# Kernel optimization log

Measured on AMD Instinct MI355X. Metric: run time of the kernel, lower is better.

## Reference

```python
import jax, jax.numpy as jnp
import numpy as np

C = 64          # num_channels
NB = 8          # num_bessel
NE = 10         # num_elements
N_NODES = 20000
N_EDGES = 320000

def _silu_norm():
    # e3nn normalize2mom constant for silu: 1/sqrt(E[silu(Z)^2]), Z~N(0,1)
    x, w = np.polynomial.hermite.hermgauss(100)
    z = np.sqrt(2.0) * x
    f = z / (1.0 + np.exp(-z))
    m2 = float(np.sum(w * f * f) / np.sqrt(np.pi))
    return np.float32(1.0 / np.sqrt(m2))

C_SILU = _silu_norm()
SQRT3 = np.float32(np.sqrt(3.0))
SQRT2 = np.float32(np.sqrt(2.0))
INV_SQRT_C = np.float32(1.0 / np.sqrt(C))
INV_SQRT_2C = np.float32(1.0 / np.sqrt(2 * C))
INV_SQRT_3C = np.float32(1.0 / np.sqrt(3 * C))
INV_SQRT_NB = np.float32(1.0 / np.sqrt(NB))
INV_SQRT_64 = np.float32(1.0 / np.sqrt(64.0))


def setup_inputs() -> dict:
    key = jax.random.key(0)
    ks = jax.random.split(key, 22)
    n = lambda k, s: jax.random.normal(k, s, dtype=jnp.float32)
    return {
        "node_feats": n(ks[0], (N_NODES, 4 * C)),
        "edge_feats": jax.random.uniform(ks[1], (N_EDGES, NB), dtype=jnp.float32),
        "edge_attrs": n(ks[2], (N_EDGES, 4)),
        "iedges": jax.random.randint(ks[3], (N_EDGES,), 0, N_NODES),
        "jedges": jax.random.randint(ks[4], (N_EDGES,), 0, N_NODES),
        "atomic_numbers": jax.random.randint(ks[5], (N_NODES,), 0, NE),
        "Wup0": n(ks[6], (C, C)), "Wup1": n(ks[7], (C, C)),
        "Wm1": n(ks[8], (NB, 64)), "Wm2": n(ks[9], (64, 64)),
        "Wm3": n(ks[10], (64, 64)), "Wm4": n(ks[11], (64, 5 * C)),
        "Wl0": n(ks[12], (2 * C, C)), "Wl1": n(ks[13], (3 * C, C)),
        "Ws0c1": n(ks[14], (NE, 1, C)), "Ws0c2": n(ks[15], (NE, 2, C)),
        "Ws0c3": n(ks[16], (NE, 2, C)),
        "Ws1c1": n(ks[17], (NE, 1, C)), "Ws1c2": n(ks[18], (NE, 1, C)),
        "Ws1c3": n(ks[19], (NE, 2, C)),
        "Wp0": n(ks[20], (C, C)), "Wp1": n(ks[21], (C, C)),
    }


def reference(node_feats, edge_feats, edge_attrs, iedges, jedges, atomic_numbers,
              Wup0, Wup1, Wm1, Wm2, Wm3, Wm4, Wl0, Wl1,
              Ws0c1, Ws0c2, Ws0c3, Ws1c1, Ws1c2, Ws1c3, Wp0, Wp1):
    Nn = node_feats.shape[0]
    # split irreps: C scalars (0e) then C vectors (1e), channel-major layout
    s = node_feats[:, :C]                       # (N, C)
    v = node_feats[:, C:].reshape(Nn, C, 3)     # (N, C, 3)

    # linear_up: per-l channel mixing, fan-in normalized (e3nn o3.Linear)
    s = (s @ Wup0) * INV_SQRT_C
    v = jnp.einsum('ncm,ck->nkm', v, Wup1) * INV_SQRT_C

    # conv_tp_weights: e3nn FullyConnectedNet [8,64,64,64,5C] with silu
    h = jax.nn.silu(edge_feats @ (Wm1 * INV_SQRT_NB)) * C_SILU
    h = jax.nn.silu(h @ (Wm2 * INV_SQRT_64)) * C_SILU
    h = jax.nn.silu(h @ (Wm3 * INV_SQRT_64)) * C_SILU
    tpw = h @ (Wm4 * INV_SQRT_64)               # (E, 5C)

    # gather sender node features per edge
    xs = s[iedges]                              # (E, C)
    xv = v[iedges]                              # (E, C, 3)
    eas = edge_attrs[:, 0:1]                    # (E, 1) scalar edge attr
    eav = edge_attrs[:, 1:4]                    # (E, 3) vector edge attr

    # 5 uvu CG paths (component-normalized e3nn TensorProduct):
    wa, wb = tpw[:, 0:C], tpw[:, C:2 * C]
    wc, wd, we = tpw[:, 2 * C:3 * C], tpw[:, 3 * C:4 * C], tpw[:, 4 * C:5 * C]
    m0 = wa * xs * eas                                              # 0e x 0e -> 0e
    m1 = wb * jnp.einsum('ecm,em->ec', xv, eav) / SQRT3             # 1e x 1e -> 0e
    m2 = (wc * xs)[:, :, None] * eav[:, None, :]                    # 0e x 1e -> 1e
    m3 = (wd * eas)[:, :, None] * xv                                # 1e x 0e -> 1e
    m4 = we[:, :, None] * jnp.cross(xv, eav[:, None, :]) / SQRT2    # 1e x 1e -> 1e

    # scatter-sum messages to receiver nodes
    msg_s = jax.ops.segment_sum(jnp.concatenate([m0, m1], axis=1), jedges, num_segments=Nn)        # (N, 2C)
    msg_v = jax.ops.segment_sum(jnp.concatenate([m2, m3, m4], axis=1), jedges, num_segments=Nn)    # (N, 3C, 3)

    # linear: middle irreps (2C x 0e + 3C x 1e) -> C x (0e + 1e)
    s2 = (msg_s @ Wl0) * INV_SQRT_2C            # (N, C)
    v2 = jnp.einsum('ncm,ck->nkm', msg_v, Wl1) * INV_SQRT_3C  # (N, C, 3)

    # symmetric (ACE/MACE) contraction, correlation=3, element-dependent weights
    w01 = Ws0c1[atomic_numbers, 0]              # (N, C)
    w02 = Ws0c2[atomic_numbers]                 # (N, 2, C)
    w03 = Ws0c3[atomic_numbers]                 # (N, 2, C)
    w11 = Ws1c1[atomic_numbers, 0]
    w12 = Ws1c2[atomic_numbers, 0]
    w13 = Ws1c3[atomic_numbers]
    vv = jnp.sum(v2 * v2, axis=-1)              # (N, C) = |v|^2 per channel
    out_s = (w01 * s2 + w02[:, 0] * s2 * s2 + w02[:, 1] * vv / SQRT3
             + w03[:, 0] * s2 * s2 * s2 + w03[:, 1] * s2 * vv / SQRT3)
    coef_v = w11 + w12 * s2 + w13[:, 0] * s2 * s2 + w13[:, 1] * vv / SQRT3
    out_v = coef_v[:, :, None] * v2             # (N, C, 3)

    # linearproduct
    so = (out_s @ Wp0) * INV_SQRT_C
    vo = jnp.einsum('ncm,ck->nkm', out_v, Wp1) * INV_SQRT_C
    return jnp.concatenate([so, vo.reshape(Nn, 3 * C)], axis=1)   # (N, 4C)
```

## Files before the change

### kernel.cpp

```cpp
#include <hip/hip_runtime.h>


typedef unsigned short u16;
typedef unsigned int u32;
typedef __attribute__((ext_vector_type(8))) short bf16x8;
typedef __attribute__((ext_vector_type(4))) float f32x4;

#define CW_UP0 0
#define CW_UP1 4096
#define CW_M1  8192
#define CW_M2  8704
#define CW_M3  12800
#define CW_M4  16896
#define CW_L0  37376
#define CW_L1  45568
#define CW_P0  57856
#define CW_P1  61952
#define CW_S01 66048
#define CW_S02 66688
#define CW_S03 67968
#define CW_S11 69248
#define CW_S12 69888
#define CW_S13 70528
#define CW_TOTAL 71808

#define C_SILU     1.6765224f
#define INV_SQRT3  0.57735027f
#define INV_SQRT2  0.70710678f
#define SC_L1      0.35355339f
#define SC_L234    0.125f

#define HSTRIDE 68
#define NFRAG   60

__device__ __forceinline__ float b2f(u16 u) {
  union { u32 i; float f; } x; x.i = ((u32)u) << 16; return x.f;
}
__device__ __forceinline__ u16 f2b(float f) {
  union { float f; u32 i; } x; x.f = f;
  u32 i = x.i;
  u32 r = (i + 0x7fffu + ((i >> 16) & 1u)) >> 16;
  return (u16)r;
}
__device__ __forceinline__ u32 pack2(float a, float b) {
  return (u32)f2b(a) | ((u32)f2b(b) << 16);
}
__device__ __forceinline__ u32 pack_hl(float y) {
  u16 h = f2b(y);
  float r = y - b2f(h);
  u16 lo = f2b(r);
  return ((u32)h << 16) | (u32)lo;
}
__device__ __forceinline__ float ldf(const void* p, size_t i, int f32) {
  return f32 ? ((const float*)p)[i] : b2f(((const u16*)p)[i]);
}
__device__ __forceinline__ float silu_n(float x) {
  return C_SILU * x / (1.0f + __expf(-x));
}
__device__ __forceinline__ bf16x8 as_bf16x8(uint4 v) {
  union { uint4 u; bf16x8 b; } x; x.u = v; return x.b;
}

__global__ void k_detect(const void* nf, int* flag) {
  __shared__ int cnt;
  if (threadIdx.x == 0) cnt = 0;
  __syncthreads();
  const u16* p = (const u16*)nf;
  int wild = 0;
  for (int i = threadIdx.x; i < 4096; i += 256) {
    float ax = fabsf(b2f(p[i]));
    if (!(ax <= 1e10f) || (ax != 0.f && ax < 1e-10f)) wild++;
  }
  atomicAdd(&cnt, wild);
  __syncthreads();
  if (threadIdx.x == 0) *flag = (cnt > 100) ? 1 : 0;
}

struct WPtrs { const void* p[16]; };

__global__ __launch_bounds__(256) void k_prep(WPtrs wp, float* __restrict__ cw,
                                              const int* __restrict__ flagp) {
  const int   sizes[16]  = {4096,4096,512,4096,4096,20480,8192,12288,4096,4096,
                            640,1280,1280,640,640,1280};
  const float scales[16] = {0.125f,0.125f,0.35355339f,0.125f,0.125f,0.125f,
                            0.08838835f,0.07216878f,0.125f,0.125f,
                            1.f,1.f,1.f,1.f,1.f,1.f};
  const int f32 = *flagp;
  int gid = blockIdx.x * 256 + threadIdx.x;
  if (gid >= CW_TOTAL) return;
  int off = gid, seg = 0;
  while (off >= sizes[seg]) { off -= sizes[seg]; seg++; }
  cw[gid] = ldf(wp.p[seg], off, f32) * scales[seg];
}

__global__ __launch_bounds__(256) void k_prepB(
    const void* __restrict__ wm1, const void* __restrict__ wm2,
    const void* __restrict__ wm3, const void* __restrict__ wm4,
    u16* __restrict__ bwH, u16* __restrict__ bwL,
    const int* __restrict__ flagp) {
  const int f32 = *flagp;
  int gid = blockIdx.x * 256 + threadIdx.x;
  if (gid >= NFRAG * 512) return;
  int f = gid >> 9, idx = gid & 511;
  int l = idx >> 3, j = idx & 7;
  int q = l >> 4, col16 = l & 15;
  float v = 0.f;
  if (f < 4) {
    int k = q * 8 + j, n = f * 16 + col16;
    if (k < 8) v = ldf(wm1, (size_t)k * 64 + n, f32);
  } else if (f < 20) {
    const void* w = (f < 12) ? wm2 : wm3;
    int t = (f < 12) ? f - 4 : f - 12;
    int n = (t >> 1) * 16 + col16, ks = t & 1;
    int k = ks * 32 + q * 8 + j;
    v = ldf(w, (size_t)k * 64 + n, f32);
  } else {
    int t = f - 20;
    int n = (t >> 1) * 16 + col16, ks = t & 1;
    int k = ks * 32 + q * 8 + j;
    v = ldf(wm4, (size_t)k * 320 + n, f32);
  }
  u16 hi = f2b(v);
  u16 lo = f2b(v - b2f(hi));
  size_t o = (size_t)f * 512 + (size_t)l * 8 + j;
  bwH[o] = hi;
  bwL[o] = lo;
}

__global__ __launch_bounds__(256) void k_hist(const int* __restrict__ je,
                                              int* __restrict__ deg, int nE) {
  int e = blockIdx.x * 256 + threadIdx.x;
  if (e < nE) atomicAdd(&deg[je[e]], 1);
}

__global__ __launch_bounds__(256) void k_scan(const int* __restrict__ deg,
                                              int* __restrict__ offs,
                                              int* __restrict__ cursor, int nN) {
  __shared__ int part[256];
  int t = threadIdx.x;
  int per = (nN + 255) / 256;
  int lo = t * per, hi = (t + 1) * per; if (hi > nN) hi = nN;
  int s = 0;
  for (int i = lo; i < hi; i++) s += deg[i];
  part[t] = s;
  __syncthreads();
  if (t == 0) {
    int run = 0;
    for (int i = 0; i < 256; i++) { int v = part[i]; part[i] = run; run += v; }
    offs[nN] = run;
  }
  __syncthreads();
  int run = part[t];
  for (int i = lo; i < hi; i++) {
    offs[i] = run; cursor[i] = run; run += deg[i];
  }
}

__global__ __launch_bounds__(256) void k_scatter(const int* __restrict__ je,
                                                 int* __restrict__ cursor,
                                                 int* __restrict__ eidx, int nE) {
  int e = blockIdx.x * 256 + threadIdx.x;
  if (e < nE) {
    int pos = atomicAdd(&cursor[je[e]], 1);
    eidx[pos] = e;
  }
}

__global__ __launch_bounds__(256) void k_node_up(
    const void* __restrict__ nf, const float* __restrict__ cw,
    float* __restrict__ sup, float* __restrict__ vup, int nN,
    const int* __restrict__ flagp) {
  __shared__ float row[4][256];
  const int f32 = *flagp;
  int w = threadIdx.x >> 6, l = threadIdx.x & 63;
  int n = blockIdx.x * 4 + w;
  bool valid = n < nN;
  int nn = valid ? n : 0;
#pragma unroll
  for (int t = 0; t < 4; t++)
    row[w][t * 64 + l] = ldf(nf, (size_t)nn * 256 + t * 64 + l, f32);
  __syncthreads();
  float sacc = 0.f, v0 = 0.f, v1 = 0.f, v2 = 0.f;
#pragma unroll 8
  for (int c = 0; c < 64; c++) {
    float w0 = cw[CW_UP0 + c * 64 + l];
    float w1 = cw[CW_UP1 + c * 64 + l];
    sacc += row[w][c] * w0;
    v0 += row[w][64 + c * 3 + 0] * w1;
    v1 += row[w][64 + c * 3 + 1] * w1;
    v2 += row[w][64 + c * 3 + 2] * w1;
  }
  if (valid) {
    sup[(size_t)n * 64 + l] = sacc;
    vup[((size_t)n * 3 + 0) * 64 + l] = v0;
    vup[((size_t)n * 3 + 1) * 64 + l] = v1;
    vup[((size_t)n * 3 + 2) * 64 + l] = v2;
  }
}

__global__ __launch_bounds__(192) void k_mlp3(
    const void* __restrict__ ef, const int* __restrict__ eidx,
    const int* __restrict__ offs, const u16* __restrict__ bwH,
    const u16* __restrict__ bwL, u16* __restrict__ tpw,
    int gn0, int gn1, int capEff, const int* __restrict__ flagp) {
  __shared__ u32 H[3][64 * HSTRIDE];
  const int f32 = *flagp;
  int tid = threadIdx.x;
  int w = tid >> 6, l = tid & 63;
  int m = l & 15, q = l >> 4;
  int base = offs[gn0];
  int cnt = offs[gn1] - base;
  int lim = cnt < capEff ? cnt : capEff;
  int tb = (blockIdx.x * 3 + w) * 64;
  if (tb >= lim) return;
  u32* Hw = H[w];

  bf16x8 zero8 = {0,0,0,0,0,0,0,0};
  bf16x8 A1h[4], A1l[4];
#pragma unroll
  for (int t = 0; t < 4; t++) { A1h[t] = zero8; A1l[t] = zero8; }
  if (q == 0) {
#pragma unroll
    for (int t = 0; t < 4; t++) {
      int s = tb + t * 16 + m; if (s > lim - 1) s = lim - 1;
      int eid = eidx[base + s];
      if (f32) {
        const float4* p = (const float4*)ef;
        float4 q0 = p[(size_t)eid * 2], q1 = p[(size_t)eid * 2 + 1];
        float v[8] = {q0.x, q0.y, q0.z, q0.w, q1.x, q1.y, q1.z, q1.w};
        bf16x8 hi, lo;
#pragma unroll
        for (int j = 0; j < 8; j++) {
          u16 h = f2b(v[j]);
          hi[j] = (short)h;
          lo[j] = (short)f2b(v[j] - b2f(h));
        }
        A1h[t] = hi; A1l[t] = lo;
      } else {
        uint4 r = ((const uint4*)ef)[eid];
        A1h[t] = as_bf16x8(r);
      }
    }
  }
#pragma unroll
  for (int n = 0; n < 4; n++) {
    bf16x8 Bh = *(const bf16x8*)(bwH + (size_t)n * 512 + (size_t)l * 8);
    bf16x8 Bl = *(const bf16x8*)(bwL + (size_t)n * 512 + (size_t)l * 8);
#pragma unroll
    for (int t = 0; t < 4; t++) {
      f32x4 c = (f32x4){0.f, 0.f, 0.f, 0.f};
      c = __builtin_amdgcn_mfma_f32_16x16x32_bf16(A1h[t], Bh, c, 0, 0, 0);
      c = __builtin_amdgcn_mfma_f32_16x16x32_bf16(A1l[t], Bh, c, 0, 0, 0);
      c = __builtin_amdgcn_mfma_f32_16x16x32_bf16(A1h[t], Bl, c, 0, 0, 0);
#pragma unroll
      for (int r = 0; r < 4; r++) {
        float y = silu_n(c[r] * SC_L1);
        Hw[(t * 16 + q * 4 + r) * HSTRIDE + n * 16 + m] = pack_hl(y);
      }
    }
  }

#pragma unroll
  for (int layer = 0; layer < 2; layer++) {
    int fragBase = 4 + layer * 8;
    bf16x8 Ah[2][4], Al[2][4];
#pragma unroll
    for (int ks = 0; ks < 2; ks++)
#pragma unroll
      for (int t = 0; t < 4; t++) {
        const uint4* hp =
            (const uint4*)(Hw + (t * 16 + m) * HSTRIDE + ks * 32 + q * 8);
        uint4 v0 = hp[0], v1 = hp[1];
        u32 raw[8] = {v0.x, v0.y, v0.z, v0.w, v1.x, v1.y, v1.z, v1.w};
        bf16x8 hi, lo;
#pragma unroll
        for (int j = 0; j < 8; j++) {
          hi[j] = (short)(raw[j] >> 16);
          lo[j] = (short)(raw[j] & 0xffffu);
        }
        Ah[ks][t] = hi; Al[ks][t] = lo;
      }
#pragma unroll
    for (int n = 0; n < 4; n++) {
      bf16x8 B0h = *(const bf16x8*)(bwH + (size_t)(fragBase + n * 2 + 0) * 512 +
                                    (size_t)l * 8);
      bf16x8 B0l = *(const bf16x8*)(bwL + (size_t)(fragBase + n * 2 + 0) * 512 +
                                    (size_t)l * 8);
      bf16x8 B1h = *(const bf16x8*)(bwH + (size_t)(fragBase + n * 2 + 1) * 512 +
                                    (size_t)l * 8);
      bf16x8 B1l = *(const bf16x8*)(bwL + (size_t)(fragBase + n * 2 + 1) * 512 +
                                    (size_t)l * 8);
#pragma unroll
      for (int t = 0; t < 4; t++) {
        f32x4 c = (f32x4){0.f, 0.f, 0.f, 0.f};
        c = __builtin_amdgcn_mfma_f32_16x16x32_bf16(Ah[0][t], B0h, c, 0, 0, 0);
        c = __builtin_amdgcn_mfma_f32_16x16x32_bf16(Al[0][t], B0h, c, 0, 0, 0);
        c = __builtin_amdgcn_mfma_f32_16x16x32_bf16(Ah[0][t], B0l, c, 0, 0, 0);
        c = __builtin_amdgcn_mfma_f32_16x16x32_bf16(Ah[1][t], B1h, c, 0, 0, 0);
        c = __builtin_amdgcn_mfma_f32_16x16x32_bf16(Al[1][t], B1h, c, 0, 0, 0);
        c = __builtin_amdgcn_mfma_f32_16x16x32_bf16(Ah[1][t], B1l, c, 0, 0, 0);
#pragma unroll
        for (int r = 0; r < 4; r++) {
          float y = silu_n(c[r] * SC_L234);
          Hw[(t * 16 + q * 4 + r) * HSTRIDE + n * 16 + m] = pack_hl(y);
        }
      }
    }
  }

  {
    bf16x8 Ah[2][4], Al[2][4];
#pragma unroll
    for (int ks = 0; ks < 2; ks++)
#pragma unroll
      for (int t = 0; t < 4; t++) {
        const uint4* hp =
            (const uint4*)(Hw + (t * 16 + m) * HSTRIDE + ks * 32 + q * 8);
        uint4 v0 = hp[0], v1 = hp[1];
        u32 raw[8] = {v0.x, v0.y, v0.z, v0.w, v1.x, v1.y, v1.z, v1.w};
        bf16x8 hi, lo;
#pragma unroll
        for (int j = 0; j < 8; j++) {
          hi[j] = (short)(raw[j] >> 16);
          lo[j] = (short)(raw[j] & 0xffffu);
        }
        Ah[ks][t] = hi; Al[ks][t] = lo;
      }
    for (int n = 0; n < 20; n++) {
      bf16x8 B0h = *(const bf16x8*)(bwH + (size_t)(20 + n * 2 + 0) * 512 +
                                    (size_t)l * 8);
      bf16x8 B0l = *(const bf16x8*)(bwL + (size_t)(20 + n * 2 + 0) * 512 +
                                    (size_t)l * 8);
      bf16x8 B1h = *(const bf16x8*)(bwH + (size_t)(20 + n * 2 + 1) * 512 +
                                    (size_t)l * 8);
      bf16x8 B1l = *(const bf16x8*)(bwL + (size_t)(20 + n * 2 + 1) * 512 +
                                    (size_t)l * 8);
#pragma unroll
      for (int t = 0; t < 4; t++) {
        f32x4 c = (f32x4){0.f, 0.f, 0.f, 0.f};
        c = __builtin_amdgcn_mfma_f32_16x16x32_bf16(Ah[0][t], B0h, c, 0, 0, 0);
        c = __builtin_amdgcn_mfma_f32_16x16x32_bf16(Al[0][t], B0h, c, 0, 0, 0);
        c = __builtin_amdgcn_mfma_f32_16x16x32_bf16(Ah[0][t], B0l, c, 0, 0, 0);
        c = __builtin_amdgcn_mfma_f32_16x16x32_bf16(Ah[1][t], B1h, c, 0, 0, 0);
        c = __builtin_amdgcn_mfma_f32_16x16x32_bf16(Al[1][t], B1h, c, 0, 0, 0);
        c = __builtin_amdgcn_mfma_f32_16x16x32_bf16(Ah[1][t], B1l, c, 0, 0, 0);
#pragma unroll
        for (int r = 0; r < 4; r++) {
          int srow = tb + t * 16 + q * 4 + r;
          if (srow < lim)
            tpw[(size_t)srow * 320 + n * 16 + m] = f2b(c[r] * SC_L234);
        }
      }
    }
  }
}

__global__ __launch_bounds__(256) void k_gather3(
    const void* __restrict__ ea, const int* __restrict__ ie,
    const int* __restrict__ offs, const int* __restrict__ eidx,
    const float* __restrict__ sup, const float* __restrict__ vup,
    const int* __restrict__ an, const float* __restrict__ cw,
    const u16* __restrict__ tpw, void* __restrict__ out, int nN,
    int gn0, int gn1, int capEff, const int* __restrict__ flagp) {
  __shared__ float B[4][960];
  const int f32 = *flagp;
  int w = threadIdx.x >> 6, l = threadIdx.x & 63;
  int n = gn0 + blockIdx.x * 4 + w;
  bool valid = n < gn1;
  int nn = valid ? n : gn0;
  int gbase = offs[gn0];
  int start = offs[nn];
  int deg = offs[nn + 1] - start;
  int avail = capEff - (start - gbase);
  int dmax = deg < avail ? deg : avail;
  if (dmax < 0) dmax = 0;

  float as0 = 0.f, as1 = 0.f;
  float av[9];
#pragma unroll
  for (int m = 0; m < 9; m++) av[m] = 0.f;

  for (int qq = 0; qq < dmax; qq++) {
    int s = start + qq;
    int ee = __builtin_amdgcn_readfirstlane(eidx[s]);
    int i  = __builtin_amdgcn_readfirstlane(ie[ee]);
    const u16* tp = tpw + (size_t)(s - gbase) * 320;
    float wa  = b2f(tp[l]);
    float wbv = b2f(tp[64 + l]);
    float wc  = b2f(tp[128 + l]);
    float wd  = b2f(tp[192 + l]);
    float we_ = b2f(tp[256 + l]);
    float eas, ev0, ev1, ev2;
    if (f32) {
      const float4 r = ((const float4*)ea)[ee];
      eas = r.x; ev0 = r.y; ev1 = r.z; ev2 = r.w;
    } else {
      uint2 r = ((const uint2*)ea)[ee];
      eas = b2f(r.x & 0xffff); ev0 = b2f(r.x >> 16);
      ev1 = b2f(r.y & 0xffff); ev2 = b2f(r.y >> 16);
    }
    float xs  = sup[(size_t)i * 64 + l];
    float xv0 = vup[((size_t)i * 3 + 0) * 64 + l];
    float xv1 = vup[((size_t)i * 3 + 1) * 64 + l];
    float xv2 = vup[((size_t)i * 3 + 2) * 64 + l];
    float dot = xv0 * ev0 + xv1 * ev1 + xv2 * ev2;
    as0 += wa * xs * eas;
    as1 += wbv * dot * INV_SQRT3;
    float wcxs = wc * xs;
    float wde  = wd * eas;
    float wef  = we_ * INV_SQRT2;
    av[0] += wcxs * ev0; av[1] += wcxs * ev1; av[2] += wcxs * ev2;
    av[3] += wde * xv0;  av[4] += wde * xv1;  av[5] += wde * xv2;
    av[6] += wef * (xv1 * ev2 - xv2 * ev1);
    av[7] += wef * (xv2 * ev0 - xv0 * ev2);
    av[8] += wef * (xv0 * ev1 - xv1 * ev0);
  }

  float* Bb = B[w];
  Bb[l] = as0;
  Bb[64 + l] = as1;
#pragma unroll
  for (int m = 0; m < 3; m++) {
    Bb[128 + l * 3 + m] = av[m];
    Bb[320 + l * 3 + m] = av[3 + m];
    Bb[512 + l * 3 + m] = av[6 + m];
  }
  __syncthreads();

  float s2 = 0.f;
#pragma unroll 8
  for (int c = 0; c < 128; c++) s2 += Bb[c] * cw[CW_L0 + c * 64 + l];
  float v20 = 0.f, v21 = 0.f, v22 = 0.f;
#pragma unroll 8
  for (int c = 0; c < 192; c++) {
    float wk = cw[CW_L1 + c * 64 + l];
    v20 += Bb[128 + c * 3 + 0] * wk;
    v21 += Bb[128 + c * 3 + 1] * wk;
    v22 += Bb[128 + c * 3 + 2] * wk;
  }
  int a = an[nn];
  float w01  = cw[CW_S01 + a * 64 + l];
  float w02a = cw[CW_S02 + a * 128 + l];
  float w02b = cw[CW_S02 + a * 128 + 64 + l];
  float w03a = cw[CW_S03 + a * 128 + l];
  float w03b = cw[CW_S03 + a * 128 + 64 + l];
  float w11  = cw[CW_S11 + a * 64 + l];
  float w12  = cw[CW_S12 + a * 64 + l];
  float w13a = cw[CW_S13 + a * 128 + l];
  float w13b = cw[CW_S13 + a * 128 + 64 + l];

  float vv = v20 * v20 + v21 * v21 + v22 * v22;
  float s2sq = s2 * s2;
  float vvs = vv * INV_SQRT3;
  float outs = w01 * s2 + w02a * s2sq + w02b * vvs + w03a * s2sq * s2 +
               w03b * s2 * vvs;
  float coef = w11 + w12 * s2 + w13a * s2sq + w13b * vvs;

  __syncthreads();
  Bb[704 + l] = outs;
  Bb[768 + l * 3 + 0] = coef * v20;
  Bb[768 + l * 3 + 1] = coef * v21;
  Bb[768 + l * 3 + 2] = coef * v22;
  __syncthreads();

  float so = 0.f, vo0 = 0.f, vo1 = 0.f, vo2 = 0.f;
#pragma unroll 8
  for (int c = 0; c < 64; c++) {
    float w0 = cw[CW_P0 + c * 64 + l];
    float w1 = cw[CW_P1 + c * 64 + l];
    so  += Bb[704 + c] * w0;
    vo0 += Bb[768 + c * 3 + 0] * w1;
    vo1 += Bb[768 + c * 3 + 1] * w1;
    vo2 += Bb[768 + c * 3 + 2] * w1;
  }
  if (valid) {
    size_t basep = (size_t)n * 256;
    if (f32) {
      float* o = (float*)out;
      o[basep + l] = so;
      o[basep + 64 + l * 3 + 0] = vo0;
      o[basep + 64 + l * 3 + 1] = vo1;
      o[basep + 64 + l * 3 + 2] = vo2;
    } else {
      u16* o = (u16*)out;
      o[basep + l] = f2b(so);
      o[basep + 64 + l * 3 + 0] = f2b(vo0);
      o[basep + 64 + l * 3 + 1] = f2b(vo1);
      o[basep + 64 + l * 3 + 2] = f2b(vo2);
    }
  }
}

extern "C" void kernel_launch(void* const* d_in, const int* in_sizes, int n_in,
                              void* d_out, int out_size, void* d_ws,
                              size_t ws_size, hipStream_t stream) {
  const void* nf = d_in[0];
  const void* ef = d_in[1];
  const void* ea = d_in[2];
  const int* ie = (const int*)d_in[3];
  const int* je = (const int*)d_in[4];
  const int* an = (const int*)d_in[5];
  int nN = in_sizes[0] / 256;
  int nE = in_sizes[3];

  size_t intCnt = (size_t)3 * nN + 1 + nE;
  intCnt = (intCnt + 3) & ~(size_t)3;
  int* deg    = (int*)d_ws;
  int* offs   = deg + nN;
  int* cursor = offs + nN + 1;
  int* eidx   = cursor + nN;
  float* cw   = (float*)d_ws + intCnt;
  float* sup  = cw + CW_TOTAL;
  float* vup  = sup + (size_t)nN * 64;
  int* flag   = (int*)(vup + (size_t)nN * 192);

  size_t bwByte = (intCnt + CW_TOTAL + (size_t)nN * 256 + 1) * 4;
  bwByte = (bwByte + 15) & ~(size_t)15;
  u16* bwH = (u16*)((char*)d_ws + bwByte);
  u16* bwL = bwH + (size_t)NFRAG * 512;
  size_t tpwByte = bwByte + (size_t)NFRAG * 512 * 2 * 2;
  tpwByte = (tpwByte + 15) & ~(size_t)15;
  u16* tpw = (u16*)((char*)d_ws + tpwByte);
  size_t capE = (ws_size > tpwByte) ? (ws_size - tpwByte) / 640 : 0;

  int G = 64;
  int nodesPer = (nN + 63) / 64;
  for (int g = 1; g <= 64; g++) {
    int npg = (nN + g - 1) / g;
    size_t worst = (size_t)npg * nE / nN + 6000;
    if (worst <= capE) { G = g; nodesPer = npg; break; }
  }
  int capEff = (int)((size_t)nodesPer * nE / nN + 6000);
  if ((size_t)capEff > capE) capEff = (int)capE;

  k_detect<<<1, 256, 0, stream>>>(nf, flag);
  hipMemsetAsync(deg, 0, (size_t)nN * sizeof(int), stream);

  WPtrs wp;
  const int widx[16] = {6, 7, 8, 9, 10, 11, 12, 13, 20, 21,
                        14, 15, 16, 17, 18, 19};
  for (int i = 0; i < 16; i++) wp.p[i] = d_in[widx[i]];
  k_prep<<<(CW_TOTAL + 255) / 256, 256, 0, stream>>>(wp, cw, flag);
  k_prepB<<<(NFRAG * 512 + 255) / 256, 256, 0, stream>>>(
      d_in[8], d_in[9], d_in[10], d_in[11], bwH, bwL, flag);

  k_hist<<<(nE + 255) / 256, 256, 0, stream>>>(je, deg, nE);
  k_scan<<<1, 256, 0, stream>>>(deg, offs, cursor, nN);
  k_scatter<<<(nE + 255) / 256, 256, 0, stream>>>(je, cursor, eidx, nE);
  k_node_up<<<(nN + 3) / 4, 256, 0, stream>>>(nf, cw, sup, vup, nN, flag);

  int mlp3Blocks = (capEff + 191) / 192;
  for (int g = 0; g < G; g++) {
    int gn0 = g * nodesPer;
    if (gn0 >= nN) break;
    int gn1 = gn0 + nodesPer; if (gn1 > nN) gn1 = nN;
    k_mlp3<<<mlp3Blocks, 192, 0, stream>>>(ef, eidx, offs, bwH, bwL, tpw,
                                           gn0, gn1, capEff, flag);
    int gBlocks = (gn1 - gn0 + 3) / 4;
    k_gather3<<<gBlocks, 256, 0, stream>>>(ea, ie, offs, eidx, sup, vup, an,
                                           cw, tpw, d_out, nN, gn0, gn1,
                                           capEff, flag);
  }
}
```

Before: 507.5 us.

## Fuse front-end prep kernels and split each node's edge gather across four waves

Merges the weight prep, B-fragment prep, degree histogram and node up-projection into one launch with block-range dispatch, cutting several kernel launches. The up-projection now reads raw weights directly and applies the scale itself, so it no longer depends on the prepared weight buffer. The gather kernel now assigns one node per block and spreads that node's edges over four waves, prefetching the next edge index, then reduces the partials through shared memory. This adds more parallelism per node for high-degree nodes, at the cost of an extra reduction and redundant tail work in the waves other than wave 0.

```diff
diff --git a/kernel.cpp b/kernel.cpp
--- a/kernel.cpp
+++ b/kernel.cpp
@@ -42,9 +42,6 @@
   u32 r = (i + 0x7fffu + ((i >> 16) & 1u)) >> 16;
   return (u16)r;
 }
-__device__ __forceinline__ u32 pack2(float a, float b) {
-  return (u32)f2b(a) | ((u32)f2b(b) << 16);
-}
 __device__ __forceinline__ u32 pack_hl(float y) {
   u16 h = f2b(y);
   float r = y - b2f(h);
@@ -78,59 +75,82 @@
 
 struct WPtrs { const void* p[16]; };
 
-__global__ __launch_bounds__(256) void k_prep(WPtrs wp, float* __restrict__ cw,
-                                              const int* __restrict__ flagp) {
-  const int   sizes[16]  = {4096,4096,512,4096,4096,20480,8192,12288,4096,4096,
-                            640,1280,1280,640,640,1280};
-  const float scales[16] = {0.125f,0.125f,0.35355339f,0.125f,0.125f,0.125f,
-                            0.08838835f,0.07216878f,0.125f,0.125f,
-                            1.f,1.f,1.f,1.f,1.f,1.f};
+__global__ __launch_bounds__(256) void k_front(
+    WPtrs wp, float* __restrict__ cw, u16* __restrict__ bwH,
+    u16* __restrict__ bwL, const int* __restrict__ je, int* __restrict__ deg,
+    const void* __restrict__ nf, float* __restrict__ sup,
+    float* __restrict__ vup, int nN, int nE, int nb0,
+    const int* __restrict__ flagp) {
+  __shared__ float row[4][256];
   const int f32 = *flagp;
-  int gid = blockIdx.x * 256 + threadIdx.x;
-  if (gid >= CW_TOTAL) return;
-  int off = gid, seg = 0;
-  while (off >= sizes[seg]) { off -= sizes[seg]; seg++; }
-  cw[gid] = ldf(wp.p[seg], off, f32) * scales[seg];
-}
-
-__global__ __launch_bounds__(256) void k_prepB(
-    const void* __restrict__ wm1, const void* __restrict__ wm2,
-    const void* __restrict__ wm3, const void* __restrict__ wm4,
-    u16* __restrict__ bwH, u16* __restrict__ bwL,
-    const int* __restrict__ flagp) {
-  const int f32 = *flagp;
-  int gid = blockIdx.x * 256 + threadIdx.x;
-  if (gid >= NFRAG * 512) return;
-  int f = gid >> 9, idx = gid & 511;
-  int l = idx >> 3, j = idx & 7;
-  int q = l >> 4, col16 = l & 15;
-  float v = 0.f;
-  if (f < 4) {
-    int k = q * 8 + j, n = f * 16 + col16;
-    if (k < 8) v = ldf(wm1, (size_t)k * 64 + n, f32);
-  } else if (f < 20) {
-    const void* w = (f < 12) ? wm2 : wm3;
-    int t = (f < 12) ? f - 4 : f - 12;
-    int n = (t >> 1) * 16 + col16, ks = t & 1;
-    int k = ks * 32 + q * 8 + j;
-    v = ldf(w, (size_t)k * 64 + n, f32);
+  int bid = blockIdx.x, tid = threadIdx.x;
+
+  if (bid < 281) {
+    const int   sizes[16]  = {4096,4096,512,4096,4096,20480,8192,12288,4096,
+                              4096,640,1280,1280,640,640,1280};
+    const float scales[16] = {0.125f,0.125f,0.35355339f,0.125f,0.125f,0.125f,
+                              0.08838835f,0.07216878f,0.125f,0.125f,
+                              1.f,1.f,1.f,1.f,1.f,1.f};
+    int gid = bid * 256 + tid;
+    if (gid >= CW_TOTAL) return;
+    int off = gid, seg = 0;
+    while (off >= sizes[seg]) { off -= sizes[seg]; seg++; }
+    cw[gid] = ldf(wp.p[seg], off, f32) * scales[seg];
+  } else if (bid < 401) {
+    int gid = (bid - 281) * 256 + tid;
+    int f = gid >> 9, idx = gid & 511;
+    int l = idx >> 3, j = idx & 7;
+    int q = l >> 4, col16 = l & 15;
+    float v = 0.f;
+    if (f < 4) {
+      int k = q * 8 + j, n = f * 16 + col16;
+      if (k < 8) v = ldf(wp.p[2], (size_t)k * 64 + n, f32);
+    } else if (f < 20) {
+      const void* w = (f < 12) ? wp.p[3] : wp.p[4];
+      int t = (f < 12) ? f - 4 : f - 12;
+      int n = (t >> 1) * 16 + col16, ks = t & 1;
+      int k = ks * 32 + q * 8 + j;
+      v = ldf(w, (size_t)k * 64 + n, f32);
+    } else {
+      int t = f - 20;
+      int n = (t >> 1) * 16 + col16, ks = t & 1;
+      int k = ks * 32 + q * 8 + j;
+      v = ldf(wp.p[5], (size_t)k * 320 + n, f32);
+    }
+    u16 hi = f2b(v);
+    u16 lo = f2b(v - b2f(hi));
+    size_t o = (size_t)f * 512 + (size_t)l * 8 + j;
+    bwH[o] = hi;
+    bwL[o] = lo;
+  } else if (bid < nb0) {
+    int e = (bid - 401) * 256 + tid;
+    if (e < nE) atomicAdd(&deg[je[e]], 1);
   } else {
-    int t = f - 20;
-    int n = (t >> 1) * 16 + col16, ks = t & 1;
-    int k = ks * 32 + q * 8 + j;
-    v = ldf(wm4, (size_t)k * 320 + n, f32);
-  }
-  u16 hi = f2b(v);
-  u16 lo = f2b(v - b2f(hi));
-  size_t o = (size_t)f * 512 + (size_t)l * 8 + j;
-  bwH[o] = hi;
-  bwL[o] = lo;
-}
-
-__global__ __launch_bounds__(256) void k_hist(const int* __restrict__ je,
-                                              int* __restrict__ deg, int nE) {
-  int e = blockIdx.x * 256 + threadIdx.x;
-  if (e < nE) atomicAdd(&deg[je[e]], 1);
+    int w = tid >> 6, l = tid & 63;
+    int n = (bid - nb0) * 4 + w;
+    bool valid = n < nN;
+    int nn = valid ? n : 0;
+#pragma unroll
+    for (int t = 0; t < 4; t++)
+      row[w][t * 64 + l] = ldf(nf, (size_t)nn * 256 + t * 64 + l, f32);
+    __syncthreads();
+    float sacc = 0.f, v0 = 0.f, v1 = 0.f, v2 = 0.f;
+#pragma unroll 8
+    for (int c = 0; c < 64; c++) {
+      float w0 = ldf(wp.p[0], (size_t)c * 64 + l, f32);
+      float w1 = ldf(wp.p[1], (size_t)c * 64 + l, f32);
+      sacc += row[w][c] * w0;
+      v0 += row[w][64 + c * 3 + 0] * w1;
+      v1 += row[w][64 + c * 3 + 1] * w1;
+      v2 += row[w][64 + c * 3 + 2] * w1;
+    }
+    if (valid) {
+      sup[(size_t)n * 64 + l] = sacc * 0.125f;
+      vup[((size_t)n * 3 + 0) * 64 + l] = v0 * 0.125f;
+      vup[((size_t)n * 3 + 1) * 64 + l] = v1 * 0.125f;
+      vup[((size_t)n * 3 + 2) * 64 + l] = v2 * 0.125f;
+    }
+  }
 }
 
 __global__ __launch_bounds__(256) void k_scan(const int* __restrict__ deg,
@@ -163,38 +183,6 @@
   if (e < nE) {
     int pos = atomicAdd(&cursor[je[e]], 1);
     eidx[pos] = e;
-  }
-}
-
-__global__ __launch_bounds__(256) void k_node_up(
-    const void* __restrict__ nf, const float* __restrict__ cw,
-    float* __restrict__ sup, float* __restrict__ vup, int nN,
-    const int* __restrict__ flagp) {
-  __shared__ float row[4][256];
-  const int f32 = *flagp;
-  int w = threadIdx.x >> 6, l = threadIdx.x & 63;
-  int n = blockIdx.x * 4 + w;
-  bool valid = n < nN;
-  int nn = valid ? n : 0;
-#pragma unroll
-  for (int t = 0; t < 4; t++)
-    row[w][t * 64 + l] = ldf(nf, (size_t)nn * 256 + t * 64 + l, f32);
-  __syncthreads();
-  float sacc = 0.f, v0 = 0.f, v1 = 0.f, v2 = 0.f;
-#pragma unroll 8
-  for (int c = 0; c < 64; c++) {
-    float w0 = cw[CW_UP0 + c * 64 + l];
-    float w1 = cw[CW_UP1 + c * 64 + l];
-    sacc += row[w][c] * w0;
-    v0 += row[w][64 + c * 3 + 0] * w1;
-    v1 += row[w][64 + c * 3 + 1] * w1;
-    v2 += row[w][64 + c * 3 + 2] * w1;
-  }
-  if (valid) {
-    sup[(size_t)n * 64 + l] = sacc;
-    vup[((size_t)n * 3 + 0) * 64 + l] = v0;
-    vup[((size_t)n * 3 + 1) * 64 + l] = v1;
-    vup[((size_t)n * 3 + 2) * 64 + l] = v2;
   }
 }
 
@@ -355,35 +343,39 @@
   }
 }
 
-__global__ __launch_bounds__(256) void k_gather3(
+__global__ __launch_bounds__(256) void k_gather4(
     const void* __restrict__ ea, const int* __restrict__ ie,
     const int* __restrict__ offs, const int* __restrict__ eidx,
     const float* __restrict__ sup, const float* __restrict__ vup,
     const int* __restrict__ an, const float* __restrict__ cw,
-    const u16* __restrict__ tpw, void* __restrict__ out, int nN,
-    int gn0, int gn1, int capEff, const int* __restrict__ flagp) {
-  __shared__ float B[4][960];
+    const u16* __restrict__ tpw, void* __restrict__ out,
+    int gn0, int capEff, const int* __restrict__ flagp) {
+  __shared__ float part[4][11][64];
+  __shared__ float Bb[960];
   const int f32 = *flagp;
-  int w = threadIdx.x >> 6, l = threadIdx.x & 63;
-  int n = gn0 + blockIdx.x * 4 + w;
-  bool valid = n < gn1;
-  int nn = valid ? n : gn0;
+  int tid = threadIdx.x;
+  int w = __builtin_amdgcn_readfirstlane(tid >> 6);
+  int l = tid & 63;
+  int n = gn0 + blockIdx.x;
   int gbase = offs[gn0];
-  int start = offs[nn];
-  int deg = offs[nn + 1] - start;
+  int start = offs[n];
+  int deg = offs[n + 1] - start;
   int avail = capEff - (start - gbase);
   int dmax = deg < avail ? deg : avail;
   if (dmax < 0) dmax = 0;
+  int dend = start + dmax;
 
   float as0 = 0.f, as1 = 0.f;
   float av[9];
 #pragma unroll
   for (int m = 0; m < 9; m++) av[m] = 0.f;
 
-  for (int qq = 0; qq < dmax; qq++) {
-    int s = start + qq;
-    int ee = __builtin_amdgcn_readfirstlane(eidx[s]);
-    int i  = __builtin_amdgcn_readfirstlane(ie[ee]);
+  int s0 = start + w;
+  int eeC = 0, iC = 0;
+  if (s0 < dend) { eeC = eidx[s0]; iC = ie[eeC]; }
+  for (int s = s0; s < dend; s += 4) {
+    int sn = s + 4, eeN = 0, iN = 0;
+    if (sn < dend) { eeN = eidx[sn]; iN = ie[eeN]; }
     const u16* tp = tpw + (size_t)(s - gbase) * 320;
     float wa  = b2f(tp[l]);
     float wbv = b2f(tp[64 + l]);
@@ -392,17 +384,17 @@
     float we_ = b2f(tp[256 + l]);
     float eas, ev0, ev1, ev2;
     if (f32) {
-      const float4 r = ((const float4*)ea)[ee];
+      const float4 r = ((const float4*)ea)[eeC];
       eas = r.x; ev0 = r.y; ev1 = r.z; ev2 = r.w;
     } else {
-      uint2 r = ((const uint2*)ea)[ee];
+      uint2 r = ((const uint2*)ea)[eeC];
       eas = b2f(r.x & 0xffff); ev0 = b2f(r.x >> 16);
       ev1 = b2f(r.y & 0xffff); ev2 = b2f(r.y >> 16);
     }
-    float xs  = sup[(size_t)i * 64 + l];
-    float xv0 = vup[((size_t)i * 3 + 0) * 64 + l];
-    float xv1 = vup[((size_t)i * 3 + 1) * 64 + l];
-    float xv2 = vup[((size_t)i * 3 + 2) * 64 + l];
+    float xs  = sup[(size_t)iC * 64 + l];
+    float xv0 = vup[((size_t)iC * 3 + 0) * 64 + l];
+    float xv1 = vup[((size_t)iC * 3 + 1) * 64 + l];
+    float xv2 = vup[((size_t)iC * 3 + 2) * 64 + l];
     float dot = xv0 * ev0 + xv1 * ev1 + xv2 * ev2;
     as0 += wa * xs * eas;
     as1 += wbv * dot * INV_SQRT3;
@@ -414,16 +406,22 @@
     av[6] += wef * (xv1 * ev2 - xv2 * ev1);
     av[7] += wef * (xv2 * ev0 - xv0 * ev2);
     av[8] += wef * (xv0 * ev1 - xv1 * ev0);
-  }
-
-  float* Bb = B[w];
-  Bb[l] = as0;
-  Bb[64 + l] = as1;
-#pragma unroll
-  for (int m = 0; m < 3; m++) {
-    Bb[128 + l * 3 + m] = av[m];
-    Bb[320 + l * 3 + m] = av[3 + m];
-    Bb[512 + l * 3 + m] = av[6 + m];
+    eeC = eeN; iC = iN;
+  }
+
+  part[w][0][l] = as0;
+  part[w][1][l] = as1;
+#pragma unroll
+  for (int m = 0; m < 9; m++) part[w][2 + m][l] = av[m];
+  __syncthreads();
+
+  for (int j = w; j < 11; j += 4) {
+    float sj = part[0][j][l] + part[1][j][l] + part[2][j][l] + part[3][j][l];
+    if (j == 0)      Bb[l] = sj;
+    else if (j == 1) Bb[64 + l] = sj;
+    else if (j < 5)  Bb[128 + l * 3 + (j - 2)] = sj;
+    else if (j < 8)  Bb[320 + l * 3 + (j - 5)] = sj;
+    else             Bb[512 + l * 3 + (j - 8)] = sj;
   }
   __syncthreads();
 
@@ -438,7 +436,7 @@
     v21 += Bb[128 + c * 3 + 1] * wk;
     v22 += Bb[128 + c * 3 + 2] * wk;
   }
-  int a = an[nn];
+  int a = an[n];
   float w01  = cw[CW_S01 + a * 64 + l];
   float w02a = cw[CW_S02 + a * 128 + l];
   float w02b = cw[CW_S02 + a * 128 + 64 + l];
@@ -473,7 +471,7 @@
     vo1 += Bb[768 + c * 3 + 1] * w1;
     vo2 += Bb[768 + c * 3 + 2] * w1;
   }
-  if (valid) {
+  if (w == 0) {
     size_t basep = (size_t)n * 256;
     if (f32) {
       float* o = (float*)out;
@@ -540,25 +538,24 @@
   const int widx[16] = {6, 7, 8, 9, 10, 11, 12, 13, 20, 21,
                         14, 15, 16, 17, 18, 19};
   for (int i = 0; i < 16; i++) wp.p[i] = d_in[widx[i]];
-  k_prep<<<(CW_TOTAL + 255) / 256, 256, 0, stream>>>(wp, cw, flag);
-  k_prepB<<<(NFRAG * 512 + 255) / 256, 256, 0, stream>>>(
-      d_in[8], d_in[9], d_in[10], d_in[11], bwH, bwL, flag);
-
-  k_hist<<<(nE + 255) / 256, 256, 0, stream>>>(je, deg, nE);
+
+  int histNB = (nE + 255) / 256;
+  int nb0 = 401 + histNB;
+  int nupNB = (nN + 3) / 4;
+  k_front<<<nb0 + nupNB, 256, 0, stream>>>(wp, cw, bwH, bwL, je, deg, nf,
+                                           sup, vup, nN, nE, nb0, flag);
   k_scan<<<1, 256, 0, stream>>>(deg, offs, cursor, nN);
   k_scatter<<<(nE + 255) / 256, 256, 0, stream>>>(je, cursor, eidx, nE);
-  k_node_up<<<(nN + 3) / 4, 256, 0, stream>>>(nf, cw, sup, vup, nN, flag);
-
-  int mlp3Blocks = (capEff + 191) / 192;
+
   for (int g = 0; g < G; g++) {
     int gn0 = g * nodesPer;
     if (gn0 >= nN) break;
     int gn1 = gn0 + nodesPer; if (gn1 > nN) gn1 = nN;
+    int mlp3Blocks = (capEff + 191) / 192;
     k_mlp3<<<mlp3Blocks, 192, 0, stream>>>(ef, eidx, offs, bwH, bwL, tpw,
                                            gn0, gn1, capEff, flag);
-    int gBlocks = (gn1 - gn0 + 3) / 4;
-    k_gather3<<<gBlocks, 256, 0, stream>>>(ea, ie, offs, eidx, sup, vup, an,
-                                           cw, tpw, d_out, nN, gn0, gn1,
-                                           capEff, flag);
-  }
-}
+    k_gather4<<<gn1 - gn0, 256, 0, stream>>>(ea, ie, offs, eidx, sup, vup,
+                                             an, cw, tpw, d_out, gn0, capEff,
+                                             flag);
+  }
+}
```

Result: slower. 668.2 us (+31.7%).
